# Optimization experiments

Hardware: AMD Instinct MI355X
Metric: run time of the kernel (lower is better)

Reference implementation:

```python
import jax, jax.numpy as jnp
import numpy as np

K_S = 2  # spatial order
K_T = 3  # temporal localization factor


def setup_inputs() -> dict:
    key = jax.random.key(0)
    ks = jax.random.split(key, 5)
    B, T, N = 8, 12, 250
    return {
        "history_data": jax.random.normal(ks[0], (B, T, N, 128), dtype=jnp.float32),
        "Prior": jax.random.normal(ks[1], (B, T, N, 64), dtype=jnp.float32),
        "Observed": jax.random.normal(ks[2], (B, T, N, 32), dtype=jnp.float32),
        "W_emb": jax.random.normal(ks[3], (224, 64), dtype=jnp.float32) * 0.05,
        "b_emb": jnp.zeros((64,), dtype=jnp.float32),
        "use_X": 1,
    }


def _transition(adj):
    # P = D^{-1} A : faithful to diag-embed @ adj, realized as row scaling
    rowsum = adj.sum(axis=-1) + 1e-9
    d_inv = 1.0 / rowsum
    d_inv = jnp.where(jnp.isinf(d_inv) | jnp.isnan(d_inv), 0.0, d_inv)
    return d_inv[..., :, None] * adj


def _forward(history_data, Prior, Observed, W_emb, b_emb):
    # nodevec: [B,T,N,64]
    nodevec = jnp.tanh(
        jnp.concatenate([history_data, Prior, Observed], axis=-1) @ W_emb + b_emb
    )
    # similarity: [B,T,N,N]
    sim = jax.nn.relu(jnp.einsum("btnd,btmd->btnm", nodevec, nodevec))
    # symmetric normalization D^{-1/2} S D^{-1/2}
    d = (sim.sum(axis=-1) + 1e-9) ** -0.5
    adj = d[..., :, None] * sim * d[..., None, :]
    P1 = jnp.swapaxes(_transition(adj), -2, -1)
    P2 = jnp.swapaxes(_transition(jnp.swapaxes(adj, -2, -1)), -2, -1)
    N = adj.shape[-1]
    mask = 1.0 - jnp.eye(N, dtype=adj.dtype)
    outs = []
    for g in (P1, P2):
        k1 = g
        ordered = [k1 * mask]
        for _k in range(2, K_S + 1):
            k1 = k1 @ g
            ordered.append(k1 * mask)
        for og in ordered:
            B, T, Nn, _ = og.shape
            # st_localization: tile each row K_T times along last dim
            ex = jnp.broadcast_to(og[..., None, :], (B, T, Nn, K_T, Nn))
            outs.append(ex.reshape(B, T, Nn, K_T * Nn))
    return tuple(outs)


def reference(history_data, Prior, Observed, W_emb, b_emb, use_X):
    # use_X == 1 path (fc_x_emb on concatenated features)
    return _forward(history_data, Prior, Observed, W_emb, b_emb)
```

## Files before the change

### kernel.cpp

```cpp
#include <hip/hip_runtime.h>
#include <hip/hip_bf16.h>

#define G_N 96
#define N_N 250
#define N_P 256
#define E_N 64
#define OUT_GSTRIDE (250 * 750)
#define OUT_STRIDE  (96 * 250 * 750)

typedef __attribute__((ext_vector_type(4))) float floatx4;
typedef __attribute__((ext_vector_type(8))) short shortx8;

__device__ __forceinline__ float bf2f(unsigned short u) {
    union { unsigned int i; float f; } v; v.i = ((unsigned int)u) << 16; return v.f;
}
__device__ __forceinline__ unsigned short f2bf(float f) {
    union { float f; unsigned int i; } v; v.f = f;
    unsigned int x = v.i;
    return (unsigned short)((x + 0x7fffu + ((x >> 16) & 1u)) >> 16);
}

__global__ __launch_bounds__(256) void k_embed(
    const float* __restrict__ hist, const float* __restrict__ prior,
    const float* __restrict__ obs, const float* __restrict__ Wemb,
    const float* __restrict__ bemb, unsigned short* __restrict__ nvb)
{
    __shared__ __attribute__((aligned(16))) float Xt[32][68];
    __shared__ __attribute__((aligned(16))) float Wl[32][64];
    const int t  = threadIdx.x;
    const int tx = t & 15, ty = t >> 4;
    const int rr0 = blockIdx.x * 64;
    const int g   = rr0 >> 8;
    const int n0  = rr0 & 255;

    float acc[4][4] = {};

    for (int c = 0; c < 7; ++c) {
        const float* src; int rowlen, off;
        if (c < 4)      { src = hist;  rowlen = 128; off = c << 5; }
        else if (c < 6) { src = prior; rowlen = 64;  off = (c - 4) << 5; }
        else            { src = obs;   rowlen = 32;  off = 0; }
        __syncthreads();
        {
            const int d  = t & 31;
            const int nb = t >> 5;
            #pragma unroll
            for (int p = 0; p < 8; ++p) {
                const int nl = nb + p * 8;
                const int n  = n0 + nl;
                float v = 0.0f;
                if (n < N_N) v = src[(size_t)(g * N_N + n) * rowlen + off + d];
                Xt[d][nl] = v;
            }
        }
        {
            const int e  = t & 63;
            const int db = t >> 6;
            #pragma unroll
            for (int p = 0; p < 8; ++p) {
                const int dl = db + p * 4;
                Wl[dl][e] = Wemb[(c * 32 + dl) * 64 + e];
            }
        }
        __syncthreads();
        #pragma unroll
        for (int k = 0; k < 32; ++k) {
            const float4 av = *(const float4*)&Xt[k][4 * ty];
            const float4 bv = *(const float4*)&Wl[k][4 * tx];
            const float a[4] = {av.x, av.y, av.z, av.w};
            const float b[4] = {bv.x, bv.y, bv.z, bv.w};
            #pragma unroll
            for (int r = 0; r < 4; ++r)
                #pragma unroll
                for (int cc = 0; cc < 4; ++cc)
                    acc[r][cc] = fmaf(a[r], b[cc], acc[r][cc]);
        }
    }
    #pragma unroll
    for (int r = 0; r < 4; ++r) {
        const int nl = 4 * ty + r;
        const int n  = n0 + nl;
        unsigned short* d2 = nvb + ((size_t)g * N_P + (n0 + nl)) * E_N + 4 * tx;
        #pragma unroll
        for (int cc = 0; cc < 4; ++cc) {
            float v = 0.0f;
            if (n < N_N) v = tanhf(acc[r][cc] + bemb[4 * tx + cc]);
            d2[cc] = f2bf(v);
        }
    }
}

__global__ __launch_bounds__(256) void k_sim(
    const unsigned short* __restrict__ nvb, unsigned short* __restrict__ Sb,
    float* __restrict__ rowsum)
{
    const int blk = blockIdx.x;
    const int g   = blk >> 4;
    const int i0  = (blk & 15) << 4;
    const int t    = threadIdx.x;
    const int w    = t >> 6;
    const int lane = t & 63;
    const int m = lane & 15, kg = lane >> 4;

    const shortx8* nvg = (const shortx8*)(nvb + (size_t)g * N_P * E_N);
    const shortx8 a0 = nvg[(i0 + m) * 8 + kg];
    const shortx8 a1 = nvg[(i0 + m) * 8 + 4 + kg];

    floatx4 acc[4];
    const floatx4 zero = {0.f, 0.f, 0.f, 0.f};
    #pragma unroll
    for (int tt = 0; tt < 4; ++tt) {
        const int j = (w << 6) + (tt << 4) + m;
        const shortx8 b0 = nvg[j * 8 + kg];
        const shortx8 b1 = nvg[j * 8 + 4 + kg];
        floatx4 c = zero;
        c = __builtin_amdgcn_mfma_f32_16x16x32_bf16(a0, b0, c, 0, 0, 0);
        c = __builtin_amdgcn_mfma_f32_16x16x32_bf16(a1, b1, c, 0, 0, 0);
        acc[tt] = c;
    }

    float v[4] = {0.f, 0.f, 0.f, 0.f};
    unsigned short* Sg = Sb + (size_t)g * N_P * N_P;
    #pragma unroll
    for (int tt = 0; tt < 4; ++tt) {
        #pragma unroll
        for (int r = 0; r < 4; ++r) {
            float s = acc[tt][r];
            s = s > 0.f ? s : 0.f;
            const int il = (kg << 2) + r;
            const int j  = (w << 6) + (tt << 4) + m;
            Sg[(size_t)(i0 + il) * N_P + j] = f2bf(s);
            v[r] += s;
        }
    }
    #pragma unroll
    for (int r = 0; r < 4; ++r) {
        v[r] += __shfl_xor(v[r], 1);
        v[r] += __shfl_xor(v[r], 2);
        v[r] += __shfl_xor(v[r], 4);
        v[r] += __shfl_xor(v[r], 8);
    }
    __shared__ float rs[4][16];
    if (m == 0) {
        #pragma unroll
        for (int r = 0; r < 4; ++r) rs[w][(kg << 2) + r] = v[r];
    }
    __syncthreads();
    if (t < 16) rowsum[g * N_P + i0 + t] = rs[0][t] + rs[1][t] + rs[2][t] + rs[3][t];
}

__global__ __launch_bounds__(256) void k_trans(
    const unsigned short* __restrict__ Sb, const float* __restrict__ rowsum,
    float* __restrict__ cArr, float* __restrict__ wArr)
{
    const int g = blockIdx.x;
    const int t = threadIdx.x;
    __shared__ __attribute__((aligned(16))) float dL[N_P];
    dL[t] = rsqrtf(rowsum[g * N_P + t] + 1e-9f);
    __syncthreads();
    const shortx8* row = (const shortx8*)(Sb + (size_t)g * N_P * N_P + (size_t)t * N_P);
    float a0 = 0.f, a1 = 0.f, a2 = 0.f, a3 = 0.f;
    #pragma unroll
    for (int ch = 0; ch < 32; ++ch) {
        const shortx8 sv = row[ch];
        const float4 d0 = *(const float4*)&dL[ch * 8];
        const float4 d1 = *(const float4*)&dL[ch * 8 + 4];
        a0 = fmaf(bf2f((unsigned short)sv[0]), d0.x, a0);
        a1 = fmaf(bf2f((unsigned short)sv[1]), d0.y, a1);
        a2 = fmaf(bf2f((unsigned short)sv[2]), d0.z, a2);
        a3 = fmaf(bf2f((unsigned short)sv[3]), d0.w, a3);
        a0 = fmaf(bf2f((unsigned short)sv[4]), d1.x, a0);
        a1 = fmaf(bf2f((unsigned short)sv[5]), d1.y, a1);
        a2 = fmaf(bf2f((unsigned short)sv[6]), d1.z, a2);
        a3 = fmaf(bf2f((unsigned short)sv[7]), d1.w, a3);
    }
    const float s  = (a0 + a1) + (a2 + a3);
    const float d  = dL[t];
    const float r  = 1.0f / (d * s + 1e-9f);
    const float c  = r * d;
    cArr[g * N_P + t] = c;
    wArr[g * N_P + t] = c * d;
}

__global__ __launch_bounds__(256) void k_out0(
    const unsigned short* __restrict__ Sb, const float* __restrict__ rowsum,
    const float* __restrict__ cArr, float* __restrict__ out)
{
    const int blk = blockIdx.x;
    const int g   = blk >> 4;
    const int i0  = (blk & 15) << 4;
    const int t   = threadIdx.x;
    __shared__ float cL[N_P];
    cL[t] = cArr[g * N_P + t];
    __syncthreads();
    const unsigned short* Sg = Sb + (size_t)g * N_P * N_P;
    float* o0 = out + (size_t)g * OUT_GSTRIDE;
    float* o2 = out + 2 * (size_t)OUT_STRIDE + (size_t)g * OUT_GSTRIDE;
    #pragma unroll 1
    for (int il = 0; il < 16; ++il) {
        const int i = i0 + il;
        const float dI = rsqrtf(rowsum[g * N_P + i] + 1e-9f);
        const float s  = bf2f(Sg[(size_t)i * N_P + t]);
        if (i < N_N && t < N_N) {
            const float p = (t == i) ? 0.f : dI * s * cL[t];
            const size_t base = (size_t)i * 750 + t;
            o0[base] = p; o0[base + 250] = p; o0[base + 500] = p;
            o2[base] = p; o2[base + 250] = p; o2[base + 500] = p;
        }
    }
}

__global__ __launch_bounds__(256) void k_pp(
    const unsigned short* __restrict__ Sb, const float* __restrict__ rowsum,
    const float* __restrict__ cArr, const float* __restrict__ wArr,
    float* __restrict__ out)
{
    const int blk = blockIdx.x;
    const int g   = blk >> 4;
    const int i0  = ((blk >> 2) & 3) << 6;
    const int j0  = (blk & 3) << 6;
    const int t    = threadIdx.x;
    const int w    = t >> 6;
    const int lane = t & 63;
    const int m = lane & 15, kg = lane >> 4;

    __shared__ __attribute__((aligned(16))) unsigned short As[64][40];
    __shared__ __attribute__((aligned(16))) unsigned short Bs[64][40];
    __shared__ float dRow[64], cCol[64];
    __shared__ __attribute__((aligned(16))) float wL[N_P];

    if (t < 64) dRow[t] = rsqrtf(rowsum[g * N_P + i0 + t] + 1e-9f);
    else if (t < 128) cCol[t - 64] = cArr[g * N_P + j0 + (t - 64)];
    wL[t] = wArr[g * N_P + t];

    const unsigned short* Sg = Sb + (size_t)g * N_P * N_P;

    floatx4 acc[4];
    const floatx4 zero = {0.f, 0.f, 0.f, 0.f};
    #pragma unroll
    for (int tt = 0; tt < 4; ++tt) acc[tt] = zero;

    const int sr = t >> 2, sc = t & 3;
    for (int kb = 0; kb < 8; ++kb) {
        __syncthreads();
        *(uint4*)&As[sr][sc * 8] = *(const uint4*)(Sg + (size_t)(i0 + sr) * N_P + kb * 32 + sc * 8);
        *(uint4*)&Bs[sr][sc * 8] = *(const uint4*)(Sg + (size_t)(j0 + sr) * N_P + kb * 32 + sc * 8);
        __syncthreads();
        const shortx8 a = *(const shortx8*)&As[(w << 4) + m][kg << 3];
        const float4 w0 = *(const float4*)&wL[kb * 32 + (kg << 3)];
        const float4 w1 = *(const float4*)&wL[kb * 32 + (kg << 3) + 4];
        const float wv[8] = {w0.x, w0.y, w0.z, w0.w, w1.x, w1.y, w1.z, w1.w};
        shortx8 aw;
        #pragma unroll
        for (int u = 0; u < 8; ++u)
            aw[u] = (short)f2bf(bf2f((unsigned short)a[u]) * wv[u]);
        #pragma unroll
        for (int tt = 0; tt < 4; ++tt) {
            const shortx8 b = *(const shortx8*)&Bs[(tt << 4) + m][kg << 3];
            acc[tt] = __builtin_amdgcn_mfma_f32_16x16x32_bf16(aw, b, acc[tt], 0, 0, 0);
        }
    }

    float* o1 = out + (size_t)OUT_STRIDE + (size_t)g * OUT_GSTRIDE;
    float* o3 = out + 3 * (size_t)OUT_STRIDE + (size_t)g * OUT_GSTRIDE;
    #pragma unroll
    for (int tt = 0; tt < 4; ++tt) {
        #pragma unroll
        for (int r = 0; r < 4; ++r) {
            const int iL = (w << 4) + (kg << 2) + r;
            const int jL = (tt << 4) + m;
            const int I = i0 + iL, J = j0 + jL;
            if (I < N_N && J < N_N) {
                const float q = (I == J) ? 0.f : acc[tt][r] * dRow[iL] * cCol[jL];
                const size_t base = (size_t)I * 750 + J;
                o1[base] = q; o1[base + 250] = q; o1[base + 500] = q;
                o3[base] = q; o3[base + 250] = q; o3[base + 500] = q;
            }
        }
    }
}

extern "C" void kernel_launch(void* const* d_in, const int* in_sizes, int n_in,
                              void* d_out, int out_size, void* d_ws, size_t ws_size,
                              hipStream_t stream) {
    const float* hist  = (const float*)d_in[0];
    const float* prior = (const float*)d_in[1];
    const float* obs   = (const float*)d_in[2];
    const float* Wemb  = (const float*)d_in[3];
    const float* bemb  = (const float*)d_in[4];
    float* out = (float*)d_out;

    char* p = (char*)d_ws;
    unsigned short* nvb = (unsigned short*)p; p += (size_t)G_N * N_P * E_N * 2;
    unsigned short* Sb  = (unsigned short*)p; p += (size_t)G_N * N_P * N_P * 2;
    float* rowsum = (float*)p; p += (size_t)G_N * N_P * 4;
    float* cArr   = (float*)p; p += (size_t)G_N * N_P * 4;
    float* wArr   = (float*)p; p += (size_t)G_N * N_P * 4;

    k_embed<<<dim3(G_N * N_P / 64), dim3(256), 0, stream>>>(hist, prior, obs, Wemb, bemb, nvb);
    k_sim  <<<dim3(G_N * 16),       dim3(256), 0, stream>>>(nvb, Sb, rowsum);
    k_trans<<<dim3(G_N),            dim3(256), 0, stream>>>(Sb, rowsum, cArr, wArr);
    k_out0 <<<dim3(G_N * 16),       dim3(256), 0, stream>>>(Sb, rowsum, cArr, out);
    k_pp   <<<dim3(G_N * 16),       dim3(256), 0, stream>>>(Sb, rowsum, cArr, wArr, out);
}
```

Baseline: 434.6 us.

## Fuse first-order output into k_pp, parallelize k_trans, swizzle blocks, nontemporal stores

Removes the separate k_out0 kernel by having k_pp also compute and write the first-order transition outputs from S tiles, so one kernel writes all four output tensors. k_trans goes from 96 blocks with one row per thread to one row per wavefront across 6144 blocks, using shuffle reductions to expose more parallelism. Block indices are remapped across XCDs (an 8-way interleave), and the output writes use nontemporal stores to avoid cache pollution. The cost is extra scalar S gathers in k_pp and a heavier epilogue per thread.

After: 598.1 us. 37.6% more time.

```diff
diff --git a/kernel.cpp b/kernel.cpp
--- a/kernel.cpp
+++ b/kernel.cpp
@@ -10,6 +10,7 @@
 
 typedef __attribute__((ext_vector_type(4))) float floatx4;
 typedef __attribute__((ext_vector_type(8))) short shortx8;
+typedef __attribute__((ext_vector_type(4))) short shortx4;
 
 __device__ __forceinline__ float bf2f(unsigned short u) {
     union { unsigned int i; float f; } v; v.i = ((unsigned int)u) << 16; return v.f;
@@ -153,60 +154,30 @@
     const unsigned short* __restrict__ Sb, const float* __restrict__ rowsum,
     float* __restrict__ cArr, float* __restrict__ wArr)
 {
-    const int g = blockIdx.x;
+    const int blk = (blockIdx.x & 7) * 768 + (blockIdx.x >> 3);
+    const int g  = blk >> 6;
+    const int r0 = (blk & 63) << 2;
     const int t = threadIdx.x;
+    const int w = t >> 6, lane = t & 63;
     __shared__ __attribute__((aligned(16))) float dL[N_P];
     dL[t] = rsqrtf(rowsum[g * N_P + t] + 1e-9f);
     __syncthreads();
-    const shortx8* row = (const shortx8*)(Sb + (size_t)g * N_P * N_P + (size_t)t * N_P);
-    float a0 = 0.f, a1 = 0.f, a2 = 0.f, a3 = 0.f;
-    #pragma unroll
-    for (int ch = 0; ch < 32; ++ch) {
-        const shortx8 sv = row[ch];
-        const float4 d0 = *(const float4*)&dL[ch * 8];
-        const float4 d1 = *(const float4*)&dL[ch * 8 + 4];
-        a0 = fmaf(bf2f((unsigned short)sv[0]), d0.x, a0);
-        a1 = fmaf(bf2f((unsigned short)sv[1]), d0.y, a1);
-        a2 = fmaf(bf2f((unsigned short)sv[2]), d0.z, a2);
-        a3 = fmaf(bf2f((unsigned short)sv[3]), d0.w, a3);
-        a0 = fmaf(bf2f((unsigned short)sv[4]), d1.x, a0);
-        a1 = fmaf(bf2f((unsigned short)sv[5]), d1.y, a1);
-        a2 = fmaf(bf2f((unsigned short)sv[6]), d1.z, a2);
-        a3 = fmaf(bf2f((unsigned short)sv[7]), d1.w, a3);
-    }
-    const float s  = (a0 + a1) + (a2 + a3);
-    const float d  = dL[t];
-    const float r  = 1.0f / (d * s + 1e-9f);
-    const float c  = r * d;
-    cArr[g * N_P + t] = c;
-    wArr[g * N_P + t] = c * d;
-}
-
-__global__ __launch_bounds__(256) void k_out0(
-    const unsigned short* __restrict__ Sb, const float* __restrict__ rowsum,
-    const float* __restrict__ cArr, float* __restrict__ out)
-{
-    const int blk = blockIdx.x;
-    const int g   = blk >> 4;
-    const int i0  = (blk & 15) << 4;
-    const int t   = threadIdx.x;
-    __shared__ float cL[N_P];
-    cL[t] = cArr[g * N_P + t];
-    __syncthreads();
-    const unsigned short* Sg = Sb + (size_t)g * N_P * N_P;
-    float* o0 = out + (size_t)g * OUT_GSTRIDE;
-    float* o2 = out + 2 * (size_t)OUT_STRIDE + (size_t)g * OUT_GSTRIDE;
-    #pragma unroll 1
-    for (int il = 0; il < 16; ++il) {
-        const int i = i0 + il;
-        const float dI = rsqrtf(rowsum[g * N_P + i] + 1e-9f);
-        const float s  = bf2f(Sg[(size_t)i * N_P + t]);
-        if (i < N_N && t < N_N) {
-            const float p = (t == i) ? 0.f : dI * s * cL[t];
-            const size_t base = (size_t)i * 750 + t;
-            o0[base] = p; o0[base + 250] = p; o0[base + 500] = p;
-            o2[base] = p; o2[base + 250] = p; o2[base + 500] = p;
-        }
+    const int row = r0 + w;
+    const shortx4 sv = *(const shortx4*)(Sb + (size_t)g * N_P * N_P
+                                         + (size_t)row * N_P + lane * 4);
+    const float4 dv = *(const float4*)&dL[lane * 4];
+    float a = bf2f((unsigned short)sv[0]) * dv.x
+            + bf2f((unsigned short)sv[1]) * dv.y
+            + bf2f((unsigned short)sv[2]) * dv.z
+            + bf2f((unsigned short)sv[3]) * dv.w;
+    #pragma unroll
+    for (int s = 32; s; s >>= 1) a += __shfl_xor(a, s);
+    if (lane == 0) {
+        const float d = dL[row];
+        const float r = 1.0f / (d * a + 1e-9f);
+        const float c = r * d;
+        cArr[g * N_P + row] = c;
+        wArr[g * N_P + row] = c * d;
     }
 }
 
@@ -215,7 +186,7 @@
     const float* __restrict__ cArr, const float* __restrict__ wArr,
     float* __restrict__ out)
 {
-    const int blk = blockIdx.x;
+    const int blk = (blockIdx.x & 7) * 192 + (blockIdx.x >> 3);
     const int g   = blk >> 4;
     const int i0  = ((blk >> 2) & 3) << 6;
     const int j0  = (blk & 3) << 6;
@@ -261,8 +232,26 @@
         }
     }
 
-    float* o1 = out + (size_t)OUT_STRIDE + (size_t)g * OUT_GSTRIDE;
-    float* o3 = out + 3 * (size_t)OUT_STRIDE + (size_t)g * OUT_GSTRIDE;
+    float sv[4][4];
+    float dR[4], cC[4];
+    #pragma unroll
+    for (int r = 0; r < 4; ++r) dR[r] = dRow[(w << 4) + (kg << 2) + r];
+    #pragma unroll
+    for (int tt = 0; tt < 4; ++tt) cC[tt] = cCol[(tt << 4) + m];
+    #pragma unroll
+    for (int tt = 0; tt < 4; ++tt) {
+        #pragma unroll
+        for (int r = 0; r < 4; ++r) {
+            const int I = i0 + (w << 4) + (kg << 2) + r;
+            const int J = j0 + (tt << 4) + m;
+            sv[tt][r] = (I < N_N && J < N_N) ? bf2f(Sg[(size_t)I * N_P + J]) : 0.f;
+        }
+    }
+
+    float* o0 = out + (size_t)g * OUT_GSTRIDE;
+    float* o1 = o0 + (size_t)OUT_STRIDE;
+    float* o2 = o0 + 2 * (size_t)OUT_STRIDE;
+    float* o3 = o0 + 3 * (size_t)OUT_STRIDE;
     #pragma unroll
     for (int tt = 0; tt < 4; ++tt) {
         #pragma unroll
@@ -271,10 +260,22 @@
             const int jL = (tt << 4) + m;
             const int I = i0 + iL, J = j0 + jL;
             if (I < N_N && J < N_N) {
-                const float q = (I == J) ? 0.f : acc[tt][r] * dRow[iL] * cCol[jL];
+                const float dc = dR[r] * cC[tt];
+                const float p = (I == J) ? 0.f : sv[tt][r] * dc;
+                const float q = (I == J) ? 0.f : acc[tt][r] * dc;
                 const size_t base = (size_t)I * 750 + J;
-                o1[base] = q; o1[base + 250] = q; o1[base + 500] = q;
-                o3[base] = q; o3[base + 250] = q; o3[base + 500] = q;
+                __builtin_nontemporal_store(p, o0 + base);
+                __builtin_nontemporal_store(p, o0 + base + 250);
+                __builtin_nontemporal_store(p, o0 + base + 500);
+                __builtin_nontemporal_store(q, o1 + base);
+                __builtin_nontemporal_store(q, o1 + base + 250);
+                __builtin_nontemporal_store(q, o1 + base + 500);
+                __builtin_nontemporal_store(p, o2 + base);
+                __builtin_nontemporal_store(p, o2 + base + 250);
+                __builtin_nontemporal_store(p, o2 + base + 500);
+                __builtin_nontemporal_store(q, o3 + base);
+                __builtin_nontemporal_store(q, o3 + base + 250);
+                __builtin_nontemporal_store(q, o3 + base + 500);
             }
         }
     }
@@ -299,7 +300,6 @@
 
     k_embed<<<dim3(G_N * N_P / 64), dim3(256), 0, stream>>>(hist, prior, obs, Wemb, bemb, nvb);
     k_sim  <<<dim3(G_N * 16),       dim3(256), 0, stream>>>(nvb, Sb, rowsum);
-    k_trans<<<dim3(G_N),            dim3(256), 0, stream>>>(Sb, rowsum, cArr, wArr);
-    k_out0 <<<dim3(G_N * 16),       dim3(256), 0, stream>>>(Sb, rowsum, cArr, out);
+    k_trans<<<dim3(G_N * 64),       dim3(256), 0, stream>>>(Sb, rowsum, cArr, wArr);
     k_pp   <<<dim3(G_N * 16),       dim3(256), 0, stream>>>(Sb, rowsum, cArr, wArr, out);
 }
```
